# Kernel optimization log

Hardware: AMD Instinct MI355X
Metric: run time of the kernel (lower is better)

## Reference

```python
import jax, jax.numpy as jnp
import numpy as np

DIM = 256
NH = 8
PD = DIM // 16  # DynamicPosBias pos_dim = (dim//4)//4 = 16
B_ = 256
GH = 16
GW = 16
N = GH * GW
NG = 64


def setup_inputs() -> dict:
    key = jax.random.key(0)
    ks = jax.random.split(key, 24)
    s = 0.05
    inp = {
        "q": jax.random.normal(ks[0], (B_, N, DIM), dtype=jnp.float32),
        "k": jax.random.normal(ks[1], (B_, N, DIM), dtype=jnp.float32),
        "mask": jax.random.normal(ks[2], (NG, N, N), dtype=jnp.float32),
        "q_w": jax.random.normal(ks[3], (DIM, DIM), dtype=jnp.float32) * s,
        "q_b": jnp.zeros((DIM,), jnp.float32),
        "kv_w": jax.random.normal(ks[4], (2 * DIM, DIM), dtype=jnp.float32) * s,
        "kv_b": jnp.zeros((2 * DIM,), jnp.float32),
        "proj_w": jax.random.normal(ks[5], (DIM, DIM), dtype=jnp.float32) * s,
        "proj_b": jnp.zeros((DIM,), jnp.float32),
        "pp_w": jax.random.normal(ks[6], (PD, 2), dtype=jnp.float32) * s,
        "pp_b": jnp.zeros((PD,), jnp.float32),
        "ln1_g": jnp.ones((PD,), jnp.float32),
        "ln1_b": jnp.zeros((PD,), jnp.float32),
        "l1_w": jax.random.normal(ks[7], (PD, PD), dtype=jnp.float32) * s,
        "l1_b": jnp.zeros((PD,), jnp.float32),
        "ln2_g": jnp.ones((PD,), jnp.float32),
        "ln2_b": jnp.zeros((PD,), jnp.float32),
        "l2_w": jax.random.normal(ks[8], (PD, PD), dtype=jnp.float32) * s,
        "l2_b": jnp.zeros((PD,), jnp.float32),
        "ln3_g": jnp.ones((PD,), jnp.float32),
        "ln3_b": jnp.zeros((PD,), jnp.float32),
        "l3_w": jax.random.normal(ks[9], (NH, PD), dtype=jnp.float32) * s,
        "l3_b": jnp.zeros((NH,), jnp.float32),
        "H": GH,
        "W": GW,
    }
    return inp


def _ln(x, g, b):
    m = x.mean(-1, keepdims=True)
    v = ((x - m) ** 2).mean(-1, keepdims=True)
    return (x - m) / jnp.sqrt(v + 1e-5) * g + b


def _pos_bias(H, W, pp_w, pp_b, ln1_g, ln1_b, l1_w, l1_b, ln2_g, ln2_b, l2_w, l2_b, ln3_g, ln3_b, l3_w, l3_b):
    # biases: ((2H-1)*(2W-1), 2) relative offsets
    bh = jnp.arange(1 - H, H, dtype=jnp.float32)
    bw = jnp.arange(1 - W, W, dtype=jnp.float32)
    mg = jnp.stack(jnp.meshgrid(bh, bw, indexing="ij"))  # (2, 2H-1, 2W-1)
    biases = mg.reshape(2, -1).T  # (L, 2)
    # MLP (residual=False): pos3(pos2(pos1(pos_proj(b))))
    x = biases @ pp_w.T + pp_b
    x = _ln(x, ln1_g, ln1_b)
    x = jax.nn.relu(x) @ l1_w.T + l1_b
    x = _ln(x, ln2_g, ln2_b)
    x = jax.nn.relu(x) @ l2_w.T + l2_b
    x = _ln(x, ln3_g, ln3_b)
    pos = jax.nn.relu(x) @ l3_w.T + l3_b  # (L, NH)
    # relative position index (N, N)
    ch = jnp.arange(H)
    cw = jnp.arange(W)
    coords = jnp.stack(jnp.meshgrid(ch, cw, indexing="ij")).reshape(2, -1)  # (2, N)
    rel = coords[:, :, None] - coords[:, None, :]  # (2, N, N)
    rel = rel.transpose(1, 2, 0)
    rel = rel + jnp.array([H - 1, W - 1])
    idx = rel[..., 0] * (2 * W - 1) + rel[..., 1]  # (N, N)
    rpb = pos[idx.reshape(-1)].reshape(H * W, H * W, -1)  # (N, N, NH)
    return rpb.transpose(2, 0, 1)  # (NH, N, N)


def reference(q, k, mask, q_w, q_b, kv_w, kv_b, proj_w, proj_b, pp_w, pp_b,
              ln1_g, ln1_b, l1_w, l1_b, ln2_g, ln2_b, l2_w, l2_b,
              ln3_g, ln3_b, l3_w, l3_b, H, W):
    B, n, C = q.shape
    hd = C // NH
    scale = hd ** -0.5
    qh = (q @ q_w.T + q_b).reshape(B, n, NH, hd).transpose(0, 2, 1, 3)  # (B, NH, N, hd)
    kvh = (k @ kv_w.T + kv_b).reshape(B, n, 2, NH, hd).transpose(2, 0, 3, 1, 4)
    kh, vh = kvh[0], kvh[1]
    attn = jnp.einsum("bhnd,bhmd->bhnm", qh * scale, kh)
    rpb = _pos_bias(H, W, pp_w, pp_b, ln1_g, ln1_b, l1_w, l1_b,
                    ln2_g, ln2_b, l2_w, l2_b, ln3_g, ln3_b, l3_w, l3_b)
    attn = attn + rpb[None]
    nG = mask.shape[0]
    attn = attn.reshape(B // nG, nG, NH, n, n) + mask[None, :, None]
    attn = jax.nn.softmax(attn.reshape(B, NH, n, n), axis=-1)
    x = jnp.einsum("bhnm,bhmd->bhnd", attn, vh).transpose(0, 2, 1, 3).reshape(B, n, C)
    return x @ proj_w.T + proj_b
```

## Files before the change

kernel.cpp:

```cpp
#include <hip/hip_runtime.h>
#include <hip/hip_bf16.h>
#include <cstdint>
#include <cstddef>

typedef __bf16 bf16x8 __attribute__((ext_vector_type(8)));
typedef __bf16 bf16x4 __attribute__((ext_vector_type(4)));
typedef float floatx4 __attribute__((ext_vector_type(4)));

__device__ __forceinline__ floatx4 mfma16x16x32(bf16x8 a, bf16x8 b, floatx4 c) {
    return __builtin_amdgcn_mfma_f32_16x16x32_bf16(a, b, c, 0, 0, 0);
}

__device__ __forceinline__ bool flag_is_f32(const void* ones) {
    return *(const unsigned int*)ones == 0x3F800000u;
}
__device__ __forceinline__ float ld1(const void* p, int i, bool f32) {
    return f32 ? ((const float*)p)[i] : (float)((const __bf16*)p)[i];
}
__device__ __forceinline__ bf16x8 ld8(const void* p, size_t i, bool f32) {
    if (f32) {
        const float* f = (const float*)p + i;
        float4 a = *(const float4*)f;
        float4 b = *(const float4*)(f + 4);
        bf16x8 v;
        v[0] = (__bf16)a.x; v[1] = (__bf16)a.y; v[2] = (__bf16)a.z; v[3] = (__bf16)a.w;
        v[4] = (__bf16)b.x; v[5] = (__bf16)b.y; v[6] = (__bf16)b.z; v[7] = (__bf16)b.w;
        return v;
    }
    return *(const bf16x8*)((const __bf16*)p + i);
}

__device__ __forceinline__ void ln16(float* x, const void* g, const void* b, bool f32) {
    float m = 0.f;
    for (int j = 0; j < 16; ++j) m += x[j];
    m *= (1.f / 16.f);
    float v = 0.f;
    for (int j = 0; j < 16; ++j) { float d = x[j] - m; v += d * d; }
    v *= (1.f / 16.f);
    float inv = rsqrtf(v + 1e-5f);
    for (int j = 0; j < 16; ++j)
        x[j] = (x[j] - m) * inv * ld1(g, j, f32) + ld1(b, j, f32);
}

__global__ void __launch_bounds__(1024) k_pos(
    const void* __restrict__ pp_w, const void* __restrict__ pp_b,
    const void* __restrict__ g1, const void* __restrict__ b1,
    const void* __restrict__ w1, const void* __restrict__ c1,
    const void* __restrict__ g2, const void* __restrict__ b2,
    const void* __restrict__ w2, const void* __restrict__ c2,
    const void* __restrict__ g3, const void* __restrict__ b3,
    const void* __restrict__ w3, const void* __restrict__ c3,
    float* __restrict__ pos)
{
    const bool f32 = flag_is_f32(g1);
    int i = threadIdx.x;
    if (i >= 961) return;
    float by = (float)(i / 31) - 15.f;
    float bx = (float)(i % 31) - 15.f;
    float x[16], y[16];
    for (int o = 0; o < 16; ++o)
        x[o] = by * ld1(pp_w, 2 * o, f32) + bx * ld1(pp_w, 2 * o + 1, f32) + ld1(pp_b, o, f32);
    ln16(x, g1, b1, f32);
    for (int o = 0; o < 16; ++o) {
        float s = ld1(c1, o, f32);
        for (int j = 0; j < 16; ++j) s += fmaxf(x[j], 0.f) * ld1(w1, o * 16 + j, f32);
        y[o] = s;
    }
    ln16(y, g2, b2, f32);
    for (int o = 0; o < 16; ++o) {
        float s = ld1(c2, o, f32);
        for (int j = 0; j < 16; ++j) s += fmaxf(y[j], 0.f) * ld1(w2, o * 16 + j, f32);
        x[o] = s;
    }
    ln16(x, g3, b3, f32);
    for (int hh = 0; hh < 8; ++hh) {
        float s = ld1(c3, hh, f32);
        for (int j = 0; j < 16; ++j) s += fmaxf(x[j], 0.f) * ld1(w3, hh * 16 + j, f32);
        pos[i * 8 + hh] = s;
    }
}

__global__ void __launch_bounds__(256) k_rpbT(const float* __restrict__ pos,
                                              __bf16* __restrict__ rpbT)
{
    int idx = blockIdx.x * 256 + threadIdx.x;
    int i = idx & 255;
    int j = (idx >> 8) & 255;
    int h = idx >> 16;
    int dy = (i >> 4) - (j >> 4) + 15;
    int dx = (i & 15) - (j & 15) + 15;
    rpbT[idx] = (__bf16)pos[(dy * 31 + dx) * 8 + h];
}

__global__ void __launch_bounds__(256) k_maskT(const void* __restrict__ mask,
                                               __bf16* __restrict__ maskT,
                                               const void* __restrict__ flag)
{
    __shared__ float sT[64][65];
    const bool f32 = flag_is_f32(flag);
    const int g = blockIdx.x;
    const int tl = blockIdx.y;
    const int i0 = (tl & 3) * 64, j0 = (tl >> 2) * 64;
    const size_t gbase = (size_t)g * 65536;
    __bf16* mo = maskT + gbase;
    const int t = threadIdx.x;
    for (int n = 0; n < 16; ++n) {
        int e = n * 256 + t;
        int r = e >> 6, c = e & 63;
        sT[r][c] = ld1(mask, (int)(gbase + (size_t)(i0 + r) * 256 + j0 + c), f32);
    }
    __syncthreads();
    for (int n = 0; n < 16; ++n) {
        int e = n * 256 + t;
        int jj = e >> 6, ii = e & 63;
        mo[(size_t)(j0 + jj) * 256 + i0 + ii] = (__bf16)sT[ii][jj];
    }
}

template <int MODE>
__global__ void __launch_bounds__(256) k_gemm(
    const void* __restrict__ A, const void* __restrict__ W,
    const void* __restrict__ bias, void* __restrict__ out0,
    __bf16* __restrict__ out1, const void* __restrict__ flag)
{
    __shared__ __bf16 sA[128 * 40];
    __shared__ __bf16 sB[128 * 40];
    const bool in_f32 = flag_is_f32(flag);
    const bool af32 = (MODE == 2) ? false : in_f32;
    const int m0 = blockIdx.x * 128;
    const int n0 = blockIdx.y * 128;
    const int t = threadIdx.x;
    const int w = t >> 6;
    const int lane = t & 63;
    const int lm = lane & 15, q = lane >> 4;

    floatx4 acc[2][8];
    for (int a_ = 0; a_ < 2; ++a_)
        for (int b_ = 0; b_ < 8; ++b_)
            for (int r = 0; r < 4; ++r) acc[a_][b_][r] = 0.f;

    for (int kc = 0; kc < 256; kc += 32) {
        for (int s = 0; s < 2; ++s) {
            int u = t + s * 256;
            int row = u >> 2, seg = u & 3;
            *(bf16x8*)&sA[row * 40 + seg * 8] =
                ld8(A, (size_t)(m0 + row) * 256 + kc + seg * 8, af32);
            *(bf16x8*)&sB[row * 40 + seg * 8] =
                ld8(W, (size_t)(n0 + row) * 256 + kc + seg * 8, in_f32);
        }
        __syncthreads();
        bf16x8 af[2], bfr[8];
        for (int rt = 0; rt < 2; ++rt)
            af[rt] = *(const bf16x8*)&sA[(w * 32 + rt * 16 + lm) * 40 + q * 8];
        for (int ct = 0; ct < 8; ++ct)
            bfr[ct] = *(const bf16x8*)&sB[(ct * 16 + lm) * 40 + q * 8];
        for (int rt = 0; rt < 2; ++rt)
            for (int ct = 0; ct < 8; ++ct)
                acc[rt][ct] = mfma16x16x32(af[rt], bfr[ct], acc[rt][ct]);
        __syncthreads();
    }

    for (int rt = 0; rt < 2; ++rt) {
        const int rbase = m0 + w * 32 + rt * 16 + q * 4;
        for (int ct = 0; ct < 8; ++ct) {
            const int gc = n0 + ct * 16 + lm;
            const float bv = ld1(bias, gc, in_f32);
            for (int r = 0; r < 4; ++r) {
                const int gr = rbase + r;
                float v = acc[rt][ct][r] + bv;
                if (MODE == 0) {
                    int b = gr >> 8, nn = gr & 255, h = gc >> 5, d = gc & 31;
                    ((__bf16*)out0)[(((size_t)(b * 8 + h)) * 256 + nn) * 32 + d] =
                        (__bf16)(v * 0.17677669529663687f);
                } else if (MODE == 1) {
                    int b = gr >> 8, nn = gr & 255;
                    if (gc < 256) {
                        int h = gc >> 5, d = gc & 31;
                        ((__bf16*)out0)[(((size_t)(b * 8 + h)) * 256 + nn) * 32 + d] = (__bf16)v;
                    } else {
                        int f = gc - 256, h = f >> 5, d = f & 31;
                        out1[(((size_t)(b * 8 + h)) * 32 + d) * 256 + nn] = (__bf16)v;
                    }
                } else {
                    if (in_f32) ((float*)out0)[(size_t)gr * 256 + gc] = v;
                    else        ((__bf16*)out0)[(size_t)gr * 256 + gc] = (__bf16)v;
                }
            }
        }
    }
}

__global__ void __launch_bounds__(256) k_attn(
    const __bf16* __restrict__ qs, const __bf16* __restrict__ ks,
    const __bf16* __restrict__ vt, const __bf16* __restrict__ maskT,
    const __bf16* __restrict__ rpbT, __bf16* __restrict__ xb)
{
    __shared__ __bf16 sK[256 * 40];
    __shared__ __bf16 sV[32 * 264];
    __shared__ __bf16 sP[4 * 16 * 136];
    const int bid = blockIdx.x;
    const int b = bid >> 3, h = bid & 7, g = b & 63;
    const int t = threadIdx.x, w = t >> 6, lane = t & 63;
    const int lm = lane & 15, q = lane >> 4;
    const size_t bh = (size_t)(b * 8 + h);
    const __bf16* qb = qs + bh * 8192;
    const __bf16* kb = ks + bh * 8192;
    const __bf16* vb = vt + bh * 8192;
    const __bf16* mT = maskT + (size_t)g * 65536;
    const __bf16* rT = rpbT + (size_t)h * 65536;

    for (int s = 0; s < 4; ++s) {
        int u = t + s * 256;
        { int row = u >> 2, seg = u & 3;
          *(bf16x8*)&sK[row * 40 + seg * 8] = *(const bf16x8*)&kb[row * 32 + seg * 8]; }
        { int row = u >> 5, seg = u & 31;
          *(bf16x8*)&sV[row * 264 + seg * 8] = *(const bf16x8*)&vb[row * 256 + seg * 8]; }
    }
    __syncthreads();

    __bf16* sPw = sP + w * (16 * 136);
    for (int rt = 0; rt < 4; ++rt) {
        const int row16 = w * 64 + rt * 16;
        const bf16x8 aq = *(const bf16x8*)&qb[(size_t)(row16 + lm) * 32 + q * 8];

        floatx4 acc[16];
        for (int ct = 0; ct < 16; ++ct)
            for (int r = 0; r < 4; ++r) acc[ct][r] = 0.f;
        for (int ct = 0; ct < 16; ++ct) {
            const bf16x8 bk = *(const bf16x8*)&sK[(ct * 16 + lm) * 40 + q * 8];
            acc[ct] = mfma16x16x32(aq, bk, acc[ct]);
        }
        for (int ct = 0; ct < 16; ++ct) {
            const int col = ct * 16 + lm;
            const bf16x4 mv = *(const bf16x4*)&mT[(size_t)col * 256 + row16 + q * 4];
            const bf16x4 rv = *(const bf16x4*)&rT[(size_t)col * 256 + row16 + q * 4];
            for (int r = 0; r < 4; ++r)
                acc[ct][r] += (float)mv[r] + (float)rv[r];
        }
        float mx[4], inv[4];
        for (int r = 0; r < 4; ++r) {
            float m = acc[0][r];
            for (int ct = 1; ct < 16; ++ct) m = fmaxf(m, acc[ct][r]);
            for (int d = 1; d < 16; d <<= 1) m = fmaxf(m, __shfl_xor(m, d));
            mx[r] = m;
        }
        for (int r = 0; r < 4; ++r) {
            float s = 0.f;
            for (int ct = 0; ct < 16; ++ct) {
                float p = __expf(acc[ct][r] - mx[r]);
                acc[ct][r] = p;
                s += p;
            }
            for (int d = 1; d < 16; d <<= 1) s += __shfl_xor(s, d);
            inv[r] = 1.f / s;
        }
        floatx4 o0, o1;
        for (int r = 0; r < 4; ++r) { o0[r] = 0.f; o1[r] = 0.f; }
        for (int half = 0; half < 2; ++half) {
            __syncthreads();
            for (int ct = 0; ct < 8; ++ct) {
                const int c = half * 8 + ct;
                for (int r = 0; r < 4; ++r)
                    sPw[(q * 4 + r) * 136 + ct * 16 + lm] = (__bf16)acc[c][r];
            }
            __syncthreads();
            for (int ksl = 0; ksl < 4; ++ksl) {
                const bf16x8 ap = *(const bf16x8*)&sPw[lm * 136 + ksl * 32 + q * 8];
                const bf16x8 bv0 =
                    *(const bf16x8*)&sV[lm * 264 + half * 128 + ksl * 32 + q * 8];
                const bf16x8 bv1 =
                    *(const bf16x8*)&sV[(16 + lm) * 264 + half * 128 + ksl * 32 + q * 8];
                o0 = mfma16x16x32(ap, bv0, o0);
                o1 = mfma16x16x32(ap, bv1, o1);
            }
        }
        for (int r = 0; r < 4; ++r) {
            const size_t row = (size_t)b * 256 + row16 + q * 4 + r;
            xb[row * 256 + h * 32 + lm]      = (__bf16)(o0[r] * inv[r]);
            xb[row * 256 + h * 32 + 16 + lm] = (__bf16)(o1[r] * inv[r]);
        }
    }
}

extern "C" void kernel_launch(void* const* d_in, const int* in_sizes, int n_in,
                              void* d_out, int out_size, void* d_ws, size_t ws_size,
                              hipStream_t stream)
{
    const void* q      = d_in[0];
    const void* k      = d_in[1];
    const void* mask   = d_in[2];
    const void* q_w    = d_in[3];
    const void* q_b    = d_in[4];
    const void* kv_w   = d_in[5];
    const void* kv_b   = d_in[6];
    const void* proj_w = d_in[7];
    const void* proj_b = d_in[8];
    const void* flag   = d_in[11];

    char* ws = (char*)d_ws;
    __bf16* qs    = (__bf16*)(ws);
    __bf16* ksb   = (__bf16*)(ws + (size_t)33554432);
    __bf16* vtb   = (__bf16*)(ws + (size_t)2 * 33554432);
    __bf16* xbuf  = (__bf16*)(ws + (size_t)3 * 33554432);
    __bf16* maskT = (__bf16*)(ws + (size_t)4 * 33554432);
    __bf16* rpbT  = (__bf16*)(ws + (size_t)4 * 33554432 + 8388608);
    float*  pos   = (float*)(ws + (size_t)4 * 33554432 + 8388608 + 1048576);

    k_pos<<<1, 1024, 0, stream>>>(
        d_in[9],  d_in[10], d_in[11], d_in[12], d_in[13], d_in[14],
        d_in[15], d_in[16], d_in[17], d_in[18], d_in[19], d_in[20],
        d_in[21], d_in[22], pos);
    k_rpbT<<<2048, 256, 0, stream>>>(pos, rpbT);
    k_maskT<<<dim3(64, 16), 256, 0, stream>>>(mask, maskT, flag);
    k_gemm<0><<<dim3(512, 2), 256, 0, stream>>>(q, q_w, q_b, qs, nullptr, flag);
    k_gemm<1><<<dim3(512, 4), 256, 0, stream>>>(k, kv_w, kv_b, ksb, vtb, flag);
    k_attn<<<2048, 256, 0, stream>>>(qs, ksb, vtb, maskT, rpbT, xbuf);
    k_gemm<2><<<dim3(512, 2), 256, 0, stream>>>(xbuf, proj_w, proj_b, d_out, nullptr, flag);
}
```

Measured before the change: 636.8 us.

## Fuse pos-bias MLP into rpbT, remap attention blocks for L2 reuse, pad sK

Merges the single-block pos-bias MLP kernel into the rpbT expansion kernel, so each thread recomputes the tiny MLP directly instead of running a serial one-block launch plus a gather. Reorders the attention grid so consecutive blocks share the same head and nearby mask groups, aiming to improve L2 reuse of the rpbT and maskT tiles. Also changes the sK row stride from 40 to 36 elements to alter LDS bank mapping. The tradeoff is redundant MLP arithmetic per element and possibly a different bank-conflict pattern from the 36 stride.

Measured after the change: 612.1 us. 3.9% less time.

```diff
diff --git a/kernel.cpp b/kernel.cpp
--- a/kernel.cpp
+++ b/kernel.cpp
@@ -42,7 +42,7 @@
         x[j] = (x[j] - m) * inv * ld1(g, j, f32) + ld1(b, j, f32);
 }
 
-__global__ void __launch_bounds__(1024) k_pos(
+__global__ void __launch_bounds__(256) k_rpbT(
     const void* __restrict__ pp_w, const void* __restrict__ pp_b,
     const void* __restrict__ g1, const void* __restrict__ b1,
     const void* __restrict__ w1, const void* __restrict__ c1,
@@ -50,46 +50,35 @@
     const void* __restrict__ w2, const void* __restrict__ c2,
     const void* __restrict__ g3, const void* __restrict__ b3,
     const void* __restrict__ w3, const void* __restrict__ c3,
-    float* __restrict__ pos)
+    __bf16* __restrict__ rpbT)
 {
     const bool f32 = flag_is_f32(g1);
-    int i = threadIdx.x;
-    if (i >= 961) return;
-    float by = (float)(i / 31) - 15.f;
-    float bx = (float)(i % 31) - 15.f;
+    const int bid = blockIdx.x;
+    const int j = bid & 255, h = bid >> 8;
+    const int i = threadIdx.x;
+    const int dy = (i >> 4) - (j >> 4) + 15;
+    const int dx = (i & 15) - (j & 15) + 15;
+    const float by = (float)(dy - 15), bx = (float)(dx - 15);
+
     float x[16], y[16];
     for (int o = 0; o < 16; ++o)
         x[o] = by * ld1(pp_w, 2 * o, f32) + bx * ld1(pp_w, 2 * o + 1, f32) + ld1(pp_b, o, f32);
     ln16(x, g1, b1, f32);
     for (int o = 0; o < 16; ++o) {
         float s = ld1(c1, o, f32);
-        for (int j = 0; j < 16; ++j) s += fmaxf(x[j], 0.f) * ld1(w1, o * 16 + j, f32);
+        for (int jj = 0; jj < 16; ++jj) s += fmaxf(x[jj], 0.f) * ld1(w1, o * 16 + jj, f32);
         y[o] = s;
     }
     ln16(y, g2, b2, f32);
     for (int o = 0; o < 16; ++o) {
         float s = ld1(c2, o, f32);
-        for (int j = 0; j < 16; ++j) s += fmaxf(y[j], 0.f) * ld1(w2, o * 16 + j, f32);
+        for (int jj = 0; jj < 16; ++jj) s += fmaxf(y[jj], 0.f) * ld1(w2, o * 16 + jj, f32);
         x[o] = s;
     }
     ln16(x, g3, b3, f32);
-    for (int hh = 0; hh < 8; ++hh) {
-        float s = ld1(c3, hh, f32);
-        for (int j = 0; j < 16; ++j) s += fmaxf(x[j], 0.f) * ld1(w3, hh * 16 + j, f32);
-        pos[i * 8 + hh] = s;
-    }
-}
-
-__global__ void __launch_bounds__(256) k_rpbT(const float* __restrict__ pos,
-                                              __bf16* __restrict__ rpbT)
-{
-    int idx = blockIdx.x * 256 + threadIdx.x;
-    int i = idx & 255;
-    int j = (idx >> 8) & 255;
-    int h = idx >> 16;
-    int dy = (i >> 4) - (j >> 4) + 15;
-    int dx = (i & 15) - (j & 15) + 15;
-    rpbT[idx] = (__bf16)pos[(dy * 31 + dx) * 8 + h];
+    float s = ld1(c3, h, f32);
+    for (int jj = 0; jj < 16; ++jj) s += fmaxf(x[jj], 0.f) * ld1(w3, h * 16 + jj, f32);
+    rpbT[(size_t)h * 65536 + (size_t)j * 256 + i] = (__bf16)s;
 }
 
 __global__ void __launch_bounds__(256) k_maskT(const void* __restrict__ mask,
@@ -195,11 +184,15 @@
     const __bf16* __restrict__ vt, const __bf16* __restrict__ maskT,
     const __bf16* __restrict__ rpbT, __bf16* __restrict__ xb)
 {
-    __shared__ __bf16 sK[256 * 40];
+    __shared__ __bf16 sK[256 * 36];
     __shared__ __bf16 sV[32 * 264];
     __shared__ __bf16 sP[4 * 16 * 136];
     const int bid = blockIdx.x;
-    const int b = bid >> 3, h = bid & 7, g = b & 63;
+    const int x = bid & 7, rr = bid >> 3;
+    const int g = x + ((rr & 7) << 3);
+    const int h = (rr >> 3) & 7;
+    const int bi = rr >> 6;
+    const int b = g + (bi << 6);
     const int t = threadIdx.x, w = t >> 6, lane = t & 63;
     const int lm = lane & 15, q = lane >> 4;
     const size_t bh = (size_t)(b * 8 + h);
@@ -212,7 +205,7 @@
     for (int s = 0; s < 4; ++s) {
         int u = t + s * 256;
         { int row = u >> 2, seg = u & 3;
-          *(bf16x8*)&sK[row * 40 + seg * 8] = *(const bf16x8*)&kb[row * 32 + seg * 8]; }
+          *(bf16x8*)&sK[row * 36 + seg * 8] = *(const bf16x8*)&kb[row * 32 + seg * 8]; }
         { int row = u >> 5, seg = u & 31;
           *(bf16x8*)&sV[row * 264 + seg * 8] = *(const bf16x8*)&vb[row * 256 + seg * 8]; }
     }
@@ -227,7 +220,7 @@
         for (int ct = 0; ct < 16; ++ct)
             for (int r = 0; r < 4; ++r) acc[ct][r] = 0.f;
         for (int ct = 0; ct < 16; ++ct) {
-            const bf16x8 bk = *(const bf16x8*)&sK[(ct * 16 + lm) * 40 + q * 8];
+            const bf16x8 bk = *(const bf16x8*)&sK[(ct * 16 + lm) * 36 + q * 8];
             acc[ct] = mfma16x16x32(aq, bk, acc[ct]);
         }
         for (int ct = 0; ct < 16; ++ct) {
@@ -304,13 +297,11 @@
     __bf16* xbuf  = (__bf16*)(ws + (size_t)3 * 33554432);
     __bf16* maskT = (__bf16*)(ws + (size_t)4 * 33554432);
     __bf16* rpbT  = (__bf16*)(ws + (size_t)4 * 33554432 + 8388608);
-    float*  pos   = (float*)(ws + (size_t)4 * 33554432 + 8388608 + 1048576);
-
-    k_pos<<<1, 1024, 0, stream>>>(
+
+    k_rpbT<<<2048, 256, 0, stream>>>(
         d_in[9],  d_in[10], d_in[11], d_in[12], d_in[13], d_in[14],
         d_in[15], d_in[16], d_in[17], d_in[18], d_in[19], d_in[20],
-        d_in[21], d_in[22], pos);
-    k_rpbT<<<2048, 256, 0, stream>>>(pos, rpbT);
+        d_in[21], d_in[22], rpbT);
     k_maskT<<<dim3(64, 16), 256, 0, stream>>>(mask, maskT, flag);
     k_gemm<0><<<dim3(512, 2), 256, 0, stream>>>(q, q_w, q_b, qs, nullptr, flag);
     k_gemm<1><<<dim3(512, 4), 256, 0, stream>>>(k, kv_w, kv_b, ksb, vtb, flag);
```
